# Kernel tuning notes

Measured on AMD Instinct MI355X. Metric: run time of the kernel, lower is better.

## Reference

```python
import jax, jax.numpy as jnp
import numpy as np

B, C, N = 2, 1024, 80
D = 3 * C + 2  # 3074 token dim
DFF = 2048     # torch TransformerEncoderLayer default dim_feedforward
HW = 224
REFINE = 3
EPS = 1e-5


def _layernorm(x, g, b):
    m = jnp.mean(x, axis=-1, keepdims=True)
    v = jnp.mean((x - m) ** 2, axis=-1, keepdims=True)
    return g * (x - m) / jnp.sqrt(v + EPS) + b


def _pos_encoding(seq_len, dim):
    pos = jnp.arange(seq_len, dtype=jnp.float32)[:, None]
    div = jnp.exp(jnp.arange(0, dim, 2, dtype=jnp.float32) * (-np.log(10000.0) / dim))
    pe = jnp.zeros((seq_len, dim), dtype=jnp.float32)
    pe = pe.at[:, 0::2].set(jnp.sin(pos * div)).at[:, 1::2].set(jnp.cos(pos * div))
    return pe


def _forward(pre_f, curr_f, first_f, ln_g, ln_b, ipw, ipb, opw, opb,
             n1g, n1b, l1w, l1b, l2w, l2b, n2g, n2b, ow, ob,
             prev_b, first_b):
    # --- vectorized find_best_shift: batched circular L1 correlation ---
    idx = (jnp.arange(N)[None, :] - jnp.arange(N)[:, None]) % N  # [shift, pos]
    rolled = first_b[:, idx]                                     # [B, N, N, 2]
    dist = jnp.abs(prev_b[:, None] - rolled).sum(axis=(-1, -2))  # [B, N]
    best = jnp.argmin(dist, axis=1)                              # first min, like torch loop
    roll_idx = (jnp.arange(N)[None, :] - best[:, None]) % N      # [B, N]
    first_b = jax.vmap(lambda fb, ri: fb[ri])(first_b, roll_idx)

    # --- bilinear upsample to 224x224 (F.interpolate, align_corners=False) ---
    up = lambda f: jax.image.resize(f, (f.shape[0], f.shape[1], HW, HW), method='bilinear')
    pre_up, curr_up, first_up = up(pre_f), up(curr_f), up(first_f)

    # --- vectorized get_bou_features: [B,N,C] gather ---
    gather = jax.vmap(lambda f, b: f[:, b[:, 0], b[:, 1]].T)
    pre_q = gather(pre_up, prev_b)      # [B, N, C]
    first_q = gather(first_up, first_b)  # [B, N, C]

    pe = _pos_encoding(N, D)
    curr = prev_b.astype(jnp.float32)
    scale = 1.0 / jnp.sqrt(jnp.float32(D))
    results = []
    for _ in range(REFINE):
        bf = gather(curr_up, curr.astype(jnp.int32))          # [B, N, C]
        tokens = jnp.concatenate([pre_q, bf, curr, first_q], axis=-1)  # [B, N, D]
        tokens = _layernorm(tokens, ln_g, ln_b)
        tokens = tokens + pe[None]
        # --- TransformerEncoderLayer (post-norm, nhead=1, relu, eval/no dropout) ---
        qkv = tokens @ ipw.T + ipb
        q, k, v = jnp.split(qkv, 3, axis=-1)
        attn = jax.nn.softmax(jnp.einsum('bqd,bkd->bqk', q, k) * scale, axis=-1)
        a = jnp.einsum('bqk,bkd->bqd', attn, v) @ opw.T + opb
        x = _layernorm(tokens + a, n1g, n1b)
        ff = jax.nn.relu(x @ l1w.T + l1b) @ l2w.T + l2b
        x = _layernorm(x + ff, n2g, n2b)
        out = x @ ow.T + ob                                   # [B, N, 1026]
        curr = jnp.clip(curr + out[..., C:], 0.0, 223.0)
        pre_q = pre_q + out[..., :C]
        results.append(curr)
    return jnp.stack(results)  # [REFINE, B, N, 2]


def setup_inputs() -> dict:
    key = jax.random.key(0)
    ks = jax.random.split(key, 12)
    f = lambda i, s: jax.random.normal(ks[i], s, dtype=jnp.float32)
    w = lambda i, s: 0.02 * jax.random.normal(ks[i], s, dtype=jnp.float32)
    return {
        'pre_img_features': f(0, (B, C, 14, 14)),
        'curr_img_features': f(1, (B, C, 14, 14)),
        'first_img_features': f(2, (B, C, 14, 14)),
        'previous_boundary': jax.random.randint(ks[3], (B, N, 2), 0, HW),
        'first_boundary': jax.random.randint(ks[4], (B, N, 2), 0, HW),
        'ln_g': jnp.ones((D,), jnp.float32), 'ln_b': jnp.zeros((D,), jnp.float32),
        'in_proj_w': w(5, (3 * D, D)), 'in_proj_b': jnp.zeros((3 * D,), jnp.float32),
        'out_proj_w': w(6, (D, D)), 'out_proj_b': jnp.zeros((D,), jnp.float32),
        'norm1_g': jnp.ones((D,), jnp.float32), 'norm1_b': jnp.zeros((D,), jnp.float32),
        'lin1_w': w(7, (DFF, D)), 'lin1_b': jnp.zeros((DFF,), jnp.float32),
        'lin2_w': w(8, (D, DFF)), 'lin2_b': jnp.zeros((D,), jnp.float32),
        'norm2_g': jnp.ones((D,), jnp.float32), 'norm2_b': jnp.zeros((D,), jnp.float32),
        'out_w': w(9, (C + 2, D)), 'out_b': jnp.zeros((C + 2,), jnp.float32),
    }


def reference(pre_img_features, curr_img_features, first_img_features,
              previous_boundary, first_boundary,
              ln_g, ln_b, in_proj_w, in_proj_b, out_proj_w, out_proj_b,
              norm1_g, norm1_b, lin1_w, lin1_b, lin2_w, lin2_b,
              norm2_g, norm2_b, out_w, out_b):
    return _forward(pre_img_features, curr_img_features, first_img_features,
                    ln_g, ln_b, in_proj_w, in_proj_b, out_proj_w, out_proj_b,
                    norm1_g, norm1_b, lin1_w, lin1_b, lin2_w, lin2_b,
                    norm2_g, norm2_b, out_w, out_b,
                    previous_boundary, first_boundary)
```

## Files before the change

### kernel.cpp

```cpp
#include <hip/hip_runtime.h>
#include <math.h>

#define B_    2
#define C_    1024
#define N_    80
#define D_    3074
#define DFF_  2048
#define OD_   1026
#define QKV_  9222
#define M_    160
#define EPS_  1e-5f
#define KPD_  3104

#define SQKV 4
#define PQKV 25
#define SOP  8
#define POP  13
#define SFF1 11
#define PFF1 9
#define SFF2 8
#define PFF2 8
#define SHD  11
#define PHD  9

typedef __attribute__((ext_vector_type(8))) short bf16x8;
typedef __attribute__((ext_vector_type(4))) float f32x4;

__device__ inline short f2bf(float f) {
    unsigned u = __float_as_uint(f);
    u += 0x7fffu + ((u >> 16) & 1u);
    return (short)(u >> 16);
}

__device__ inline int pack2bf(float lo, float hi) {
    return (int)(unsigned short)f2bf(lo) | ((int)(unsigned short)f2bf(hi) << 16);
}

__device__ inline float wave_sum(float v) {
#pragma unroll
    for (int off = 32; off > 0; off >>= 1) v += __shfl_down(v, off, 64);
    return v;
}

__device__ inline void block_reduce_2(float& s, float& s2, float* red) {
    int tid = threadIdx.x;
    int lane = tid & 63, wid = tid >> 6;
    s = wave_sum(s);
    s2 = wave_sum(s2);
    if (lane == 0) { red[wid] = s; red[4 + wid] = s2; }
    __syncthreads();
    if (tid == 0) {
        red[8] = red[0] + red[1] + red[2] + red[3];
        red[9] = red[4] + red[5] + red[6] + red[7];
    }
    __syncthreads();
    s = red[8]; s2 = red[9];
}

__device__ inline void bilin_setup(int p, int& i0, int& i1, float& t) {
    float s = (p + 0.5f) * 0.0625f - 0.5f;
    s = fminf(fmaxf(s, 0.0f), 13.0f);
    i0 = (int)s;
    t = s - (float)i0;
    i1 = min(i0 + 1, 13);
}

__device__ inline float bilin_tap(const float* f, int y0, int y1, float ty,
                                  int x0, int x1, float tx) {
    float a = f[y0 * 14 + x0], b = f[y0 * 14 + x1];
    float c = f[y1 * 14 + x0], d = f[y1 * 14 + x1];
    return (1.f - ty) * ((1.f - tx) * a + tx * b) + ty * ((1.f - tx) * c + tx * d);
}

__global__ __launch_bounds__(128) void align_kernel(const int* __restrict__ prev_b,
                                                    const int* __restrict__ first_b,
                                                    int* __restrict__ fb_al) {
    int b = blockIdx.x;
    int tid = threadIdx.x;
    __shared__ int dist[N_];
    __shared__ int bestIdx;
    if (tid < N_) {
        int s = 0;
        for (int j = 0; j < N_; ++j) {
            int src = (j - tid) % N_;
            if (src < 0) src += N_;
            int dy = prev_b[(b * N_ + j) * 2] - first_b[(b * N_ + src) * 2];
            int dx = prev_b[(b * N_ + j) * 2 + 1] - first_b[(b * N_ + src) * 2 + 1];
            s += abs(dy) + abs(dx);
        }
        dist[tid] = s;
    }
    __syncthreads();
    if (tid == 0) {
        int best = 0, bd = dist[0];
        for (int i = 1; i < N_; ++i)
            if (dist[i] < bd) { bd = dist[i]; best = i; }
        bestIdx = best;
    }
    __syncthreads();
    if (tid < N_) {
        int src = (tid - bestIdx) % N_;
        if (src < 0) src += N_;
        fb_al[(b * N_ + tid) * 2]     = first_b[(b * N_ + src) * 2];
        fb_al[(b * N_ + tid) * 2 + 1] = first_b[(b * N_ + src) * 2 + 1];
    }
}

__global__ __launch_bounds__(256) void gather_init_kernel(
        const float* __restrict__ pre_f, const float* __restrict__ first_f,
        const int* __restrict__ prev_b, const int* __restrict__ fb_al,
        float* __restrict__ pre_q, float* __restrict__ first_q,
        float* __restrict__ curr) {
    int m = blockIdx.x;
    int b = m / N_;
    int tid = threadIdx.x;
    int py = prev_b[m * 2], px = prev_b[m * 2 + 1];
    int fy = fb_al[m * 2], fx = fb_al[m * 2 + 1];
    int py0, py1, px0, px1, fy0, fy1, fx0, fx1;
    float pty, ptx, fty, ftx;
    bilin_setup(py, py0, py1, pty);
    bilin_setup(px, px0, px1, ptx);
    bilin_setup(fy, fy0, fy1, fty);
    bilin_setup(fx, fx0, fx1, ftx);
    for (int c = tid; c < C_; c += 256) {
        const float* fp = pre_f + (size_t)(b * C_ + c) * 196;
        const float* ff = first_f + (size_t)(b * C_ + c) * 196;
        pre_q[(size_t)m * C_ + c]   = bilin_tap(fp, py0, py1, pty, px0, px1, ptx);
        first_q[(size_t)m * C_ + c] = bilin_tap(ff, fy0, fy1, fty, fx0, fx1, ftx);
    }
    if (tid < 2) curr[m * 2 + tid] = (float)prev_b[m * 2 + tid];
}

__global__ __launch_bounds__(256) void pe_kernel(float* __restrict__ pe) {
    int n = blockIdx.x;
    const float negLogDivD = -logf(10000.0f) / (float)D_;
    for (int d = threadIdx.x; d < D_; d += 256) {
        int kk = d >> 1;
        float ang = (float)n * expf((float)(2 * kk) * negLogDivD);
        pe[(size_t)n * D_ + d] = (d & 1) ? cosf(ang) : sinf(ang);
    }
}

__global__ __launch_bounds__(256) void tokens_kernel(
        const float* __restrict__ curr_f, const float* __restrict__ pre_q,
        const float* __restrict__ first_q, const float* __restrict__ curr,
        const float* __restrict__ ln_g, const float* __restrict__ ln_b,
        const float* __restrict__ pe_tab,
        float* __restrict__ tokens, short* __restrict__ tokens_bf) {
    int m = blockIdx.x;
    int b = m / N_;
    int n = m % N_;
    int tid = threadIdx.x;
    __shared__ float bf[C_];
    __shared__ float red[10];

    float cy = curr[m * 2], cx = curr[m * 2 + 1];
    int iy = (int)cy, ix = (int)cx;
    int y0, y1, x0, x1;
    float ty, tx;
    bilin_setup(iy, y0, y1, ty);
    bilin_setup(ix, x0, x1, tx);
    for (int c = tid; c < C_; c += 256) {
        const float* f = curr_f + (size_t)(b * C_ + c) * 196;
        bf[c] = bilin_tap(f, y0, y1, ty, x0, x1, tx);
    }
    __syncthreads();

    float s = 0.f, s2 = 0.f;
    for (int d = tid; d < D_; d += 256) {
        float v;
        if (d < C_)            v = pre_q[(size_t)m * C_ + d];
        else if (d < 2 * C_)   v = bf[d - C_];
        else if (d == 2 * C_)  v = cy;
        else if (d == 2*C_+1)  v = cx;
        else                   v = first_q[(size_t)m * C_ + (d - 2 * C_ - 2)];
        s += v; s2 += v * v;
    }
    block_reduce_2(s, s2, red);
    float mean = s / (float)D_;
    float var = s2 / (float)D_ - mean * mean;
    float inv = rsqrtf(var + EPS_);

    for (int d = tid; d < KPD_; d += 256) {
        if (d < D_) {
            float v;
            if (d < C_)            v = pre_q[(size_t)m * C_ + d];
            else if (d < 2 * C_)   v = bf[d - C_];
            else if (d == 2 * C_)  v = cy;
            else if (d == 2*C_+1)  v = cx;
            else                   v = first_q[(size_t)m * C_ + (d - 2 * C_ - 2)];
            float ln = ln_g[d] * (v - mean) * inv + ln_b[d];
            float val = ln + pe_tab[(size_t)n * D_ + d];
            tokens[(size_t)m * D_ + d] = val;
            tokens_bf[(size_t)m * KPD_ + d] = f2bf(val);
        } else {
            tokens_bf[(size_t)m * KPD_ + d] = 0;
        }
    }
}

__global__ __launch_bounds__(256) void wpack2(const float* __restrict__ w,
                                              short* __restrict__ o,
                                              int K, int O, int nch, int ntiles) {
    int gw = (int)((blockIdx.x * 256 + threadIdx.x) >> 6);
    if (gw >= ntiles) return;
    int lane = threadIdx.x & 63;
    int strip = gw / nch, chunk = gw - strip * nch;
    int row = strip * 16 + (lane >> 2);
    int k0 = chunk * 32 + (lane & 3) * 8;
    float f[8];
    if (row < O && k0 + 8 <= K) {
        const float* src = w + (size_t)row * K + k0;
        float2 a = *(const float2*)(src);
        float2 b = *(const float2*)(src + 2);
        float2 c = *(const float2*)(src + 4);
        float2 d = *(const float2*)(src + 6);
        f[0]=a.x; f[1]=a.y; f[2]=b.x; f[3]=b.y;
        f[4]=c.x; f[5]=c.y; f[6]=d.x; f[7]=d.y;
    } else {
#pragma unroll
        for (int j = 0; j < 8; ++j) {
            int k = k0 + j;
            f[j] = (row < O && k < K) ? w[(size_t)row * K + k] : 0.f;
        }
    }
    int p0 = pack2bf(f[0], f[1]);
    int p1 = pack2bf(f[2], f[3]);
    int p2 = pack2bf(f[4], f[5]);
    int p3 = pack2bf(f[6], f[7]);
    int src = (lane & 15) * 4 + (lane >> 4);
    int4 out;
    out.x = __shfl(p0, src, 64);
    out.y = __shfl(p1, src, 64);
    out.z = __shfl(p2, src, 64);
    out.w = __shfl(p3, src, 64);
    *(int4*)(o + (size_t)gw * 512 + (size_t)lane * 8) = out;
}

template <int SW>
__global__ __launch_bounds__(512) void gemm_stage(
        const short* __restrict__ A, const short* __restrict__ Wp,
        const float* __restrict__ bias, float* __restrict__ part,
        int KpA, int nch, int O, int per) {
    int cs = blockIdx.y * per;
    int ce = min(nch, cs + per);
    if (cs >= ce) return;
    int tid = threadIdx.x;
    int lane = tid & 63, wave = tid >> 6;
    int col = lane & 15, quad = lane >> 4;
    int s0 = (blockIdx.x * 8 + wave) * SW;

    __shared__ short lbuf[2][160 * 32];

    int m0 = tid >> 2, p8 = (tid & 3) * 8;
    int m1 = (tid + 512) >> 2;
    const short* a0 = A + (size_t)m0 * KpA + p8;
    const short* a1 = A + (size_t)m1 * KpA + p8;
    bf16x8 sr0, sr1;

    f32x4 acc[SW][10];
#pragma unroll
    for (int j = 0; j < SW; ++j)
#pragma unroll
        for (int t = 0; t < 10; ++t)
#pragma unroll
            for (int r = 0; r < 4; ++r) acc[j][t][r] = 0.f;

    const short* wbase[SW];
#pragma unroll
    for (int j = 0; j < SW; ++j)
        wbase[j] = Wp + (size_t)(s0 + j) * nch * 512 + (size_t)lane * 8;
    bf16x8 wc[SW], wn[SW];

    sr0 = *(const bf16x8*)(a0 + (size_t)cs * 32);
    if (tid < 128) sr1 = *(const bf16x8*)(a1 + (size_t)cs * 32);
#pragma unroll
    for (int j = 0; j < SW; ++j)
        wc[j] = *(const bf16x8*)(wbase[j] + (size_t)cs * 512);
    *(bf16x8*)(&lbuf[0][m0 * 32 + p8]) = sr0;
    if (tid < 128) *(bf16x8*)(&lbuf[0][m1 * 32 + p8]) = sr1;
    __syncthreads();

    int cur = 0;
    for (int c = cs; c < ce; ++c) {
        bool more = (c + 1) < ce;
        if (more) {
            sr0 = *(const bf16x8*)(a0 + (size_t)(c + 1) * 32);
            if (tid < 128) sr1 = *(const bf16x8*)(a1 + (size_t)(c + 1) * 32);
#pragma unroll
            for (int j = 0; j < SW; ++j)
                wn[j] = *(const bf16x8*)(wbase[j] + (size_t)(c + 1) * 512);
        }
#pragma unroll
        for (int t = 0; t < 10; ++t) {
            bf16x8 af = *(const bf16x8*)(&lbuf[cur][t * 512 + col * 32 + quad * 8]);
#pragma unroll
            for (int j = 0; j < SW; ++j)
                acc[j][t] = __builtin_amdgcn_mfma_f32_16x16x32_bf16(af, wc[j], acc[j][t], 0, 0, 0);
        }
        if (more) {
            *(bf16x8*)(&lbuf[cur ^ 1][m0 * 32 + p8]) = sr0;
            if (tid < 128) *(bf16x8*)(&lbuf[cur ^ 1][m1 * 32 + p8]) = sr1;
        }
        __syncthreads();
#pragma unroll
        for (int j = 0; j < SW; ++j) wc[j] = wn[j];
        cur ^= 1;
    }

    float* pout = part + (size_t)blockIdx.y * M_ * O;
#pragma unroll
    for (int j = 0; j < SW; ++j) {
        int oc = (s0 + j) * 16 + col;
        if (oc < O) {
            float bv = (blockIdx.y == 0) ? bias[oc] : 0.f;
#pragma unroll
            for (int t = 0; t < 10; ++t)
#pragma unroll
                for (int r = 0; r < 4; ++r)
                    pout[(size_t)(t * 16 + quad * 4 + r) * O + oc] = acc[j][t][r] + bv;
        }
    }
}

__global__ __launch_bounds__(256) void gemm_mfma_sk(
        const short* __restrict__ A, const float* __restrict__ Wf,
        const float* __restrict__ bias, float* __restrict__ Cout,
        int K, int KpA, int O, int KC) {
    int kc0 = blockIdx.y * KC;
    if (kc0 >= K) return;
    int kend = min(K, kc0 + KC);

    int lane = threadIdx.x & 63;
    int wave = threadIdx.x >> 6;
    int col  = lane & 15;
    int quad = lane >> 4;
    int o0 = blockIdx.x * 128 + wave * 32 + col;
    int o1 = o0 + 16;
    int oc0 = min(o0, O - 1), oc1 = min(o1, O - 1);

    const float* wrow0 = Wf + (size_t)oc0 * K + quad * 8;
    const float* wrow1 = Wf + (size_t)oc1 * K + quad * 8;
    const short* abase = A + (size_t)col * KpA + quad * 8;

    f32x4 acc0[10], acc1[10];
#pragma unroll
    for (int t = 0; t < 10; ++t)
#pragma unroll
        for (int r = 0; r < 4; ++r) { acc0[t][r] = 0.f; acc1[t][r] = 0.f; }

    int nfull = (kend - kc0) >> 5;
    bf16x8 aCur[10];
    float2 wCur[8];
    if (nfull > 0) {
#pragma unroll
        for (int t = 0; t < 10; ++t)
            aCur[t] = *(const bf16x8*)(abase + (size_t)t * 16 * KpA + kc0);
#pragma unroll
        for (int j = 0; j < 4; ++j) {
            wCur[j]     = *(const float2*)(wrow0 + kc0 + 2 * j);
            wCur[4 + j] = *(const float2*)(wrow1 + kc0 + 2 * j);
        }
    }
    for (int i = 0; i < nfull; ++i) {
        bf16x8 aNxt[10];
        float2 wNxt[8];
        if (i + 1 < nfull) {
            int kn = kc0 + (i + 1) * 32;
#pragma unroll
            for (int t = 0; t < 10; ++t)
                aNxt[t] = *(const bf16x8*)(abase + (size_t)t * 16 * KpA + kn);
#pragma unroll
            for (int j = 0; j < 4; ++j) {
                wNxt[j]     = *(const float2*)(wrow0 + kn + 2 * j);
                wNxt[4 + j] = *(const float2*)(wrow1 + kn + 2 * j);
            }
        }
        bf16x8 b0, b1;
#pragma unroll
        for (int j = 0; j < 4; ++j) {
            b0[2*j] = f2bf(wCur[j].x);     b0[2*j+1] = f2bf(wCur[j].y);
            b1[2*j] = f2bf(wCur[4+j].x);   b1[2*j+1] = f2bf(wCur[4+j].y);
        }
#pragma unroll
        for (int t = 0; t < 10; ++t) {
            acc0[t] = __builtin_amdgcn_mfma_f32_16x16x32_bf16(aCur[t], b0, acc0[t], 0, 0, 0);
            acc1[t] = __builtin_amdgcn_mfma_f32_16x16x32_bf16(aCur[t], b1, acc1[t], 0, 0, 0);
        }
#pragma unroll
        for (int t = 0; t < 10; ++t) aCur[t] = aNxt[t];
#pragma unroll
        for (int j = 0; j < 8; ++j) wCur[j] = wNxt[j];
    }
    int kmain = kc0 + nfull * 32;
    if (kmain < kend) {
        bf16x8 b0, b1;
#pragma unroll
        for (int j = 0; j < 8; ++j) {
            int k = kmain + quad * 8 + j;
            b0[j] = (k < kend) ? f2bf(Wf[(size_t)oc0 * K + k]) : (short)0;
            b1[j] = (k < kend) ? f2bf(Wf[(size_t)oc1 * K + k]) : (short)0;
        }
#pragma unroll
        for (int t = 0; t < 10; ++t) {
            bf16x8 af = *(const bf16x8*)(abase + (size_t)t * 16 * KpA + kmain);
            acc0[t] = __builtin_amdgcn_mfma_f32_16x16x32_bf16(af, b0, acc0[t], 0, 0, 0);
            acc1[t] = __builtin_amdgcn_mfma_f32_16x16x32_bf16(af, b1, acc1[t], 0, 0, 0);
        }
    }
    if (o0 < O) {
        float bv = (blockIdx.y == 0) ? bias[o0] : 0.f;
#pragma unroll
        for (int t = 0; t < 10; ++t)
#pragma unroll
            for (int r = 0; r < 4; ++r)
                atomicAdd(&Cout[(size_t)(t * 16 + quad * 4 + r) * O + o0], acc0[t][r] + bv);
    }
    if (o1 < O) {
        float bv = (blockIdx.y == 0) ? bias[o1] : 0.f;
#pragma unroll
        for (int t = 0; t < 10; ++t)
#pragma unroll
            for (int r = 0; r < 4; ++r)
                atomicAdd(&Cout[(size_t)(t * 16 + quad * 4 + r) * O + o1], acc1[t][r] + bv);
    }
}

__global__ __launch_bounds__(256) void relu_cvt_kernel(const float* __restrict__ in,
                                                       int S, size_t sstr,
                                                       short* __restrict__ out,
                                                       int n) {
    int i = blockIdx.x * 256 + threadIdx.x;
    if (i < n) {
        float v = 0.f;
        for (int s = 0; s < S; ++s) v += in[(size_t)s * sstr + i];
        out[i] = f2bf(fmaxf(v, 0.f));
    }
}

__global__ __launch_bounds__(256) void qkv_cvt_kernel(const float* __restrict__ part,
                                                      int S,
                                                      short* __restrict__ q_bf,
                                                      short* __restrict__ k_bf,
                                                      short* __restrict__ v_bf) {
    int mb = blockIdx.x;
    int b = mb / 96, q = mb % 96;
    if (q >= N_) {
        for (int d = threadIdx.x; d < KPD_; d += 256)
            v_bf[((size_t)b * 96 + q) * KPD_ + d] = 0;
        return;
    }
    int m = b * N_ + q;
    for (int d = threadIdx.x; d < KPD_; d += 256) {
        short qv = 0, kv = 0, vv = 0;
        if (d < D_) {
            float qf = 0.f, kf = 0.f, vf = 0.f;
            for (int s = 0; s < S; ++s) {
                const float* p = part + (size_t)s * M_ * QKV_ + (size_t)m * QKV_;
                qf += p[d]; kf += p[D_ + d]; vf += p[2 * D_ + d];
            }
            qv = f2bf(qf); kv = f2bf(kf); vv = f2bf(vf);
        }
        q_bf[(size_t)m * KPD_ + d] = qv;
        k_bf[(size_t)m * KPD_ + d] = kv;
        v_bf[((size_t)b * 96 + q) * KPD_ + d] = vv;
    }
}

__global__ __launch_bounds__(256) void attn_sc(const short* __restrict__ q_bf,
                                               const short* __restrict__ k_bf,
                                               short* __restrict__ p_bf) {
    int bi = blockIdx.x;
    int b = bi / 5, qt = bi % 5;
    int lane = threadIdx.x & 63, wave = threadIdx.x >> 6;
    int col = lane & 15, quad = lane >> 4;
    const short* qbase = q_bf + (size_t)(b * N_ + qt * 16 + col) * KPD_ + quad * 8;
    const short* kb = k_bf + (size_t)(b * N_ + col) * KPD_ + quad * 8;

    f32x4 acc[5];
#pragma unroll
    for (int kt = 0; kt < 5; ++kt)
#pragma unroll
        for (int r = 0; r < 4; ++r) acc[kt][r] = 0.f;

    int c0 = wave * 25, c1 = min(97, c0 + 25);
    for (int c = c0; c < c1; ++c) {
        bf16x8 af = *(const bf16x8*)(qbase + (size_t)c * 32);
#pragma unroll
        for (int kt = 0; kt < 5; ++kt) {
            bf16x8 kf = *(const bf16x8*)(kb + (size_t)(kt * 16) * KPD_ + (size_t)c * 32);
            acc[kt] = __builtin_amdgcn_mfma_f32_16x16x32_bf16(af, kf, acc[kt], 0, 0, 0);
        }
    }

    __shared__ f32x4 red[4][5][64];
    __shared__ float sl[16][80];
#pragma unroll
    for (int kt = 0; kt < 5; ++kt) red[wave][kt][lane] = acc[kt];
    __syncthreads();
    float scale = rsqrtf((float)D_);
    for (int item = threadIdx.x; item < 320; item += 256) {
        int kt = item >> 6, l2 = item & 63;
        int c2 = l2 & 15, q2 = l2 >> 4;
        f32x4 v = red[0][kt][l2];
#pragma unroll
        for (int w = 1; w < 4; ++w)
#pragma unroll
            for (int r = 0; r < 4; ++r) v[r] += red[w][kt][l2][r];
#pragma unroll
        for (int r = 0; r < 4; ++r)
            sl[q2 * 4 + r][kt * 16 + c2] = v[r] * scale;
    }
    __syncthreads();

    int r = wave * 4 + (lane >> 4);
    int cb = lane & 15;
    float v[5];
    float mx = -1e30f;
#pragma unroll
    for (int i = 0; i < 5; ++i) { v[i] = sl[r][cb + 16 * i]; mx = fmaxf(mx, v[i]); }
#pragma unroll
    for (int off = 1; off < 16; off <<= 1) mx = fmaxf(mx, __shfl_xor(mx, off, 64));
    float e[5];
    float sum = 0.f;
#pragma unroll
    for (int i = 0; i < 5; ++i) { e[i] = expf(v[i] - mx); sum += e[i]; }
#pragma unroll
    for (int off = 1; off < 16; off <<= 1) sum += __shfl_xor(sum, off, 64);
    float rs = 1.0f / sum;
    size_t m96 = (size_t)(b * N_ + qt * 16 + r) * 96;
#pragma unroll
    for (int i = 0; i < 5; ++i) p_bf[m96 + cb + 16 * i] = f2bf(e[i] * rs);
    p_bf[m96 + 80 + cb] = 0;
}

__global__ __launch_bounds__(256) void av_mfma(const short* __restrict__ p_bf,
                                               const short* __restrict__ v_bf,
                                               short* __restrict__ av_bf) {
    int bi = blockIdx.x;
    int b = bi / 49, g = bi % 49;
    int lane = threadIdx.x & 63, wave = threadIdx.x >> 6;
    int dtile = g * 4 + wave;
    if (dtile >= 194) return;
    int d0 = dtile * 16;
    int col = lane & 15, quad = lane >> 4;
    const short* pbase = p_bf + (size_t)b * N_ * 96 + quad * 8;
    const short* vb = v_bf + (size_t)b * 96 * KPD_ + d0 + col;
    f32x4 acc[5];
#pragma unroll
    for (int t = 0; t < 5; ++t)
#pragma unroll
        for (int r = 0; r < 4; ++r) acc[t][r] = 0.f;
#pragma unroll
    for (int c = 0; c < 3; ++c) {
        bf16x8 bf8;
#pragma unroll
        for (int j = 0; j < 8; ++j)
            bf8[j] = vb[(size_t)(c * 32 + quad * 8 + j) * KPD_];
#pragma unroll
        for (int t = 0; t < 5; ++t) {
            bf16x8 af = *(const bf16x8*)(pbase + (size_t)(t * 16 + col) * 96 + c * 32);
            acc[t] = __builtin_amdgcn_mfma_f32_16x16x32_bf16(af, bf8, acc[t], 0, 0, 0);
        }
    }
#pragma unroll
    for (int t = 0; t < 5; ++t)
#pragma unroll
        for (int r = 0; r < 4; ++r)
            av_bf[(size_t)(b * N_ + t * 16 + quad * 4 + r) * KPD_ + d0 + col] = f2bf(acc[t][r]);
}

template <bool WF32>
__global__ __launch_bounds__(256) void ln_kernel(const float* __restrict__ xin,
                                                 int S, size_t sstr,
                                                 const float* __restrict__ res,
                                                 const float* __restrict__ g,
                                                 const float* __restrict__ bta,
                                                 float* __restrict__ outf,
                                                 short* __restrict__ outb) {
    int m = blockIdx.x;
    int tid = threadIdx.x;
    __shared__ float red[10];
    const float* xr = xin + (size_t)m * D_;
    const float* rr = res + (size_t)m * D_;
    float vv[13];
    float s = 0.f, s2 = 0.f;
#pragma unroll
    for (int i = 0; i < 13; ++i) {
        int d = tid + i * 256;
        float v = 0.f;
        if (d < D_) {
            v = rr[d];
            for (int sp = 0; sp < S; ++sp) v += xr[(size_t)sp * sstr + d];
            s += v; s2 += v * v;
        }
        vv[i] = v;
    }
    block_reduce_2(s, s2, red);
    float mean = s / (float)D_;
    float var = s2 / (float)D_ - mean * mean;
    float inv = rsqrtf(var + EPS_);
#pragma unroll
    for (int i = 0; i < 13; ++i) {
        int d = tid + i * 256;
        if (d < D_) {
            float y = g[d] * (vv[i] - mean) * inv + bta[d];
            if (WF32) outf[(size_t)m * D_ + d] = y;
            outb[(size_t)m * KPD_ + d] = f2bf(y);
        } else if (d < KPD_) {
            outb[(size_t)m * KPD_ + d] = 0;
        }
    }
}

__global__ __launch_bounds__(256) void update_kernel(const float* __restrict__ part,
                                                     int S, size_t sstr,
                                                     float* __restrict__ curr,
                                                     float* __restrict__ pre_q,
                                                     float* __restrict__ results) {
    int m = blockIdx.x;
    int tid = threadIdx.x;
    const float* pr = part + (size_t)m * OD_;
    for (int c = tid; c < C_; c += 256) {
        float v = 0.f;
        for (int s = 0; s < S; ++s) v += pr[(size_t)s * sstr + c];
        pre_q[(size_t)m * C_ + c] += v;
    }
    if (tid < 2) {
        float v = 0.f;
        for (int s = 0; s < S; ++s) v += pr[(size_t)s * sstr + C_ + tid];
        float nc = curr[m * 2 + tid] + v;
        nc = fminf(fmaxf(nc, 0.f), 223.f);
        curr[m * 2 + tid] = nc;
        results[m * 2 + tid] = nc;
    }
}

extern "C" void kernel_launch(void* const* d_in, const int* in_sizes, int n_in,
                              void* d_out, int out_size, void* d_ws, size_t ws_size,
                              hipStream_t stream) {
    const float* pre_f   = (const float*)d_in[0];
    const float* curr_f  = (const float*)d_in[1];
    const float* first_f = (const float*)d_in[2];
    const int*   prev_b  = (const int*)d_in[3];
    const int*   first_b = (const int*)d_in[4];
    const float* ln_g    = (const float*)d_in[5];
    const float* ln_b    = (const float*)d_in[6];
    const float* ipw     = (const float*)d_in[7];
    const float* ipb     = (const float*)d_in[8];
    const float* opw     = (const float*)d_in[9];
    const float* opb     = (const float*)d_in[10];
    const float* n1g     = (const float*)d_in[11];
    const float* n1b     = (const float*)d_in[12];
    const float* l1w     = (const float*)d_in[13];
    const float* l1b     = (const float*)d_in[14];
    const float* l2w     = (const float*)d_in[15];
    const float* l2b     = (const float*)d_in[16];
    const float* n2g     = (const float*)d_in[17];
    const float* n2b     = (const float*)d_in[18];
    const float* ow      = (const float*)d_in[19];
    const float* ob      = (const float*)d_in[20];
    float* outp = (float*)d_out;

    float* wf = (float*)d_ws;
    size_t off = 0;
    int*   fb_al   = (int*)(wf + off); off += 320;
    float* curr    = wf + off;         off += 320;
    float* pre_q   = wf + off;         off += (size_t)M_ * C_;
    float* first_q = wf + off;         off += (size_t)M_ * C_;
    float* tokens  = wf + off;         off += (size_t)M_ * D_;
    float* xbuf    = wf + off;         off += (size_t)M_ * D_;
    float* pe_tab  = wf + off;         off += (size_t)N_ * D_;
    short* tokens_bf = (short*)(wf + off); off += (size_t)M_ * KPD_ / 2;
    short* x_bf      = (short*)(wf + off); off += (size_t)M_ * KPD_ / 2;
    short* x2_bf     = (short*)(wf + off); off += (size_t)M_ * KPD_ / 2;
    short* av_bf     = (short*)(wf + off); off += (size_t)M_ * KPD_ / 2;
    short* ff1_bf    = (short*)(wf + off); off += (size_t)M_ * DFF_ / 2;
    short* q_bf      = (short*)(wf + off); off += (size_t)M_ * KPD_ / 2;
    short* k_bf      = (short*)(wf + off); off += (size_t)M_ * KPD_ / 2;
    short* v_bf      = (short*)(wf + off); off += (size_t)B_ * 96 * KPD_ / 2;
    short* p_bf      = (short*)(wf + off); off += (size_t)M_ * 96 / 2;
    size_t commonF = off;

    size_t o2 = commonF;
    short* ipw_p2 = (short*)(wf + o2); o2 += (size_t)592 * 97 * 256;
    short* opw_p2 = (short*)(wf + o2); o2 += (size_t)208 * 97 * 256;
    short* l1w_p2 = (short*)(wf + o2); o2 += (size_t)128 * 97 * 256;
    short* l2w_p2 = (short*)(wf + o2); o2 += (size_t)208 * 64 * 256;
    short* ow_p2  = (short*)(wf + o2); o2 += (size_t)80  * 97 * 256;
    float* gpart  = wf + o2;           o2 += (size_t)SQKV * M_ * QKV_;

    size_t o0 = commonF;
    float* qkv   = wf + o0; o0 += (size_t)M_ * QKV_;
    float* aout  = wf + o0; o0 += (size_t)M_ * D_;
    float* ff1f  = wf + o0; o0 += (size_t)M_ * DFF_;
    float* ffout = wf + o0; o0 += (size_t)M_ * D_;
    float* outb  = wf + o0; o0 += (size_t)M_ * OD_;

    int tier = (ws_size >= o2 * sizeof(float)) ? 2 : 0;
    (void)in_sizes; (void)n_in; (void)out_size;

    hipLaunchKernelGGL(align_kernel, dim3(B_), dim3(128), 0, stream,
                       prev_b, first_b, fb_al);
    hipLaunchKernelGGL(gather_init_kernel, dim3(M_), dim3(256), 0, stream,
                       pre_f, first_f, prev_b, fb_al, pre_q, first_q, curr);
    hipLaunchKernelGGL(pe_kernel, dim3(N_), dim3(256), 0, stream, pe_tab);

    if (tier == 2) {
        hipLaunchKernelGGL(wpack2, dim3(592 * 97 / 4), dim3(256), 0, stream,
                           ipw, ipw_p2, D_, QKV_, 97, 592 * 97);
        hipLaunchKernelGGL(wpack2, dim3(208 * 97 / 4), dim3(256), 0, stream,
                           opw, opw_p2, D_, D_, 97, 208 * 97);
        hipLaunchKernelGGL(wpack2, dim3(128 * 97 / 4), dim3(256), 0, stream,
                           l1w, l1w_p2, D_, DFF_, 97, 128 * 97);
        hipLaunchKernelGGL(wpack2, dim3(208 * 64 / 4), dim3(256), 0, stream,
                           l2w, l2w_p2, DFF_, D_, 64, 208 * 64);
        hipLaunchKernelGGL(wpack2, dim3(80 * 97 / 4), dim3(256), 0, stream,
                           ow, ow_p2, D_, OD_, 97, 80 * 97);
    }

    for (int it = 0; it < 3; ++it) {
        if (tier == 0) {
            hipMemsetAsync(qkv,   0, (size_t)M_ * QKV_ * 4, stream);
            hipMemsetAsync(aout,  0, (size_t)M_ * D_   * 4, stream);
            hipMemsetAsync(ff1f,  0, (size_t)M_ * DFF_ * 4, stream);
            hipMemsetAsync(ffout, 0, (size_t)M_ * D_   * 4, stream);
            hipMemsetAsync(outb,  0, (size_t)M_ * OD_  * 4, stream);
        }

        hipLaunchKernelGGL(tokens_kernel, dim3(M_), dim3(256), 0, stream,
                           curr_f, pre_q, first_q, curr, ln_g, ln_b, pe_tab,
                           tokens, tokens_bf);
        if (tier == 2)
            hipLaunchKernelGGL((gemm_stage<2>), dim3(37, SQKV), dim3(512), 0, stream,
                               tokens_bf, ipw_p2, ipb, gpart, KPD_, 97, QKV_, PQKV);
        else
            hipLaunchKernelGGL(gemm_mfma_sk, dim3(73, 6), dim3(256), 0, stream,
                               tokens_bf, ipw, ipb, qkv, D_, KPD_, QKV_, 544);
        hipLaunchKernelGGL(qkv_cvt_kernel, dim3(B_ * 96), dim3(256), 0, stream,
                           (tier == 2) ? gpart : qkv, (tier == 2) ? SQKV : 1,
                           q_bf, k_bf, v_bf);
        hipLaunchKernelGGL(attn_sc, dim3(B_ * 5), dim3(256), 0, stream,
                           q_bf, k_bf, p_bf);
        hipLaunchKernelGGL(av_mfma, dim3(98), dim3(256), 0, stream,
                           p_bf, v_bf, av_bf);
        if (tier == 2)
            hipLaunchKernelGGL((gemm_stage<2>), dim3(13, SOP), dim3(512), 0, stream,
                               av_bf, opw_p2, opb, gpart, KPD_, 97, D_, POP);
        else
            hipLaunchKernelGGL(gemm_mfma_sk, dim3(25, 10), dim3(256), 0, stream,
                               av_bf, opw, opb, aout, D_, KPD_, D_, 320);
        hipLaunchKernelGGL((ln_kernel<true>), dim3(M_), dim3(256), 0, stream,
                           (tier == 2) ? gpart : aout, (tier == 2) ? SOP : 1, (size_t)M_ * D_,
                           tokens, n1g, n1b, xbuf, x_bf);
        if (tier == 2)
            hipLaunchKernelGGL((gemm_stage<2>), dim3(8, SFF1), dim3(512), 0, stream,
                               x_bf, l1w_p2, l1b, gpart, KPD_, 97, DFF_, PFF1);
        else
            hipLaunchKernelGGL(gemm_mfma_sk, dim3(16, 17), dim3(256), 0, stream,
                               x_bf, l1w, l1b, ff1f, D_, KPD_, DFF_, 192);
        hipLaunchKernelGGL(relu_cvt_kernel, dim3((M_ * DFF_ + 255) / 256), dim3(256), 0, stream,
                           (tier == 2) ? gpart : ff1f, (tier == 2) ? SFF1 : 1, (size_t)M_ * DFF_,
                           ff1_bf, M_ * DFF_);
        if (tier == 2)
            hipLaunchKernelGGL((gemm_stage<2>), dim3(13, SFF2), dim3(512), 0, stream,
                               ff1_bf, l2w_p2, l2b, gpart, DFF_, 64, D_, PFF2);
        else
            hipLaunchKernelGGL(gemm_mfma_sk, dim3(25, 11), dim3(256), 0, stream,
                               ff1_bf, l2w, l2b, ffout, DFF_, DFF_, D_, 192);
        hipLaunchKernelGGL((ln_kernel<false>), dim3(M_), dim3(256), 0, stream,
                           (tier == 2) ? gpart : ffout, (tier == 2) ? SFF2 : 1, (size_t)M_ * D_,
                           xbuf, n2g, n2b, (float*)nullptr, x2_bf);
        if (tier == 2)
            hipLaunchKernelGGL((gemm_stage<2>), dim3(5, SHD), dim3(512), 0, stream,
                               x2_bf, ow_p2, ob, gpart, KPD_, 97, OD_, PHD);
        else
            hipLaunchKernelGGL(gemm_mfma_sk, dim3(9, 13), dim3(256), 0, stream,
                               x2_bf, ow, ob, outb, D_, KPD_, OD_, 256);
        hipLaunchKernelGGL(update_kernel, dim3(M_), dim3(256), 0, stream,
                           (tier == 2) ? gpart : outb, (tier == 2) ? SHD : 1, (size_t)M_ * OD_,
                           curr, pre_q, outp + (size_t)it * M_ * 2);
    }
}
```

Baseline: 1.022 ms.

## Fuse QKV GEMM with bf16 conversion, merge softmax and AV, retune split-K

Replaces the split-K QKV GEMM and its separate reduce/convert kernel with one non-split kernel that writes bf16 Q/K/V directly with bias. Merges the softmax-score kernel and the AV multiply into one kernel that keeps probabilities in shared memory. Retunes the split-K factors of the other GEMMs, caches token values in registers inside the layernorm kernel, and zeroes the padding once up front. The QKV GEMM now runs on only 74 blocks with full K per block, which trades split-K parallelism for fewer launches and less partial-sum traffic. The fused attention runs on only 10 blocks.

Measured after the change: 1.171 ms. +14.6%, slower.

```diff
diff --git a/kernel.cpp b/kernel.cpp
--- a/kernel.cpp
+++ b/kernel.cpp
@@ -12,16 +12,14 @@
 #define EPS_  1e-5f
 #define KPD_  3104
 
-#define SQKV 4
-#define PQKV 25
-#define SOP  8
-#define POP  13
-#define SFF1 11
-#define PFF1 9
-#define SFF2 8
-#define PFF2 8
-#define SHD  11
-#define PHD  9
+#define SOP  6
+#define POP  17
+#define SFF1 6
+#define PFF1 17
+#define SFF2 6
+#define PFF2 11
+#define SHD  6
+#define PHD  17
 
 typedef __attribute__((ext_vector_type(8))) short bf16x8;
 typedef __attribute__((ext_vector_type(4))) float f32x4;
@@ -141,6 +139,27 @@
     }
 }
 
+__global__ __launch_bounds__(64) void zero_pads(short* __restrict__ q_bf,
+                                                short* __restrict__ k_bf,
+                                                short* __restrict__ v_bf) {
+    int bi = blockIdx.x;
+    int tid = threadIdx.x;
+    if (bi < M_) {
+        int b = bi / N_, q = bi % N_;
+        int d = D_ + tid;
+        if (d < KPD_) {
+            q_bf[(size_t)bi * KPD_ + d] = 0;
+            k_bf[(size_t)bi * KPD_ + d] = 0;
+            v_bf[((size_t)b * 96 + q) * KPD_ + d] = 0;
+        }
+    } else {
+        int r = bi - M_;
+        int b = r / 16, q = 80 + (r % 16);
+        for (int d = tid; d < KPD_; d += 64)
+            v_bf[((size_t)b * 96 + q) * KPD_ + d] = 0;
+    }
+}
+
 __global__ __launch_bounds__(256) void tokens_kernel(
         const float* __restrict__ curr_f, const float* __restrict__ pre_q,
         const float* __restrict__ first_q, const float* __restrict__ curr,
@@ -166,34 +185,36 @@
     }
     __syncthreads();
 
+    float vv[13];
     float s = 0.f, s2 = 0.f;
-    for (int d = tid; d < D_; d += 256) {
-        float v;
-        if (d < C_)            v = pre_q[(size_t)m * C_ + d];
-        else if (d < 2 * C_)   v = bf[d - C_];
-        else if (d == 2 * C_)  v = cy;
-        else if (d == 2*C_+1)  v = cx;
-        else                   v = first_q[(size_t)m * C_ + (d - 2 * C_ - 2)];
-        s += v; s2 += v * v;
-    }
-    block_reduce_2(s, s2, red);
-    float mean = s / (float)D_;
-    float var = s2 / (float)D_ - mean * mean;
-    float inv = rsqrtf(var + EPS_);
-
-    for (int d = tid; d < KPD_; d += 256) {
+#pragma unroll
+    for (int i = 0; i < 13; ++i) {
+        int d = tid + i * 256;
+        float v = 0.f;
         if (d < D_) {
-            float v;
             if (d < C_)            v = pre_q[(size_t)m * C_ + d];
             else if (d < 2 * C_)   v = bf[d - C_];
             else if (d == 2 * C_)  v = cy;
             else if (d == 2*C_+1)  v = cx;
             else                   v = first_q[(size_t)m * C_ + (d - 2 * C_ - 2)];
-            float ln = ln_g[d] * (v - mean) * inv + ln_b[d];
+            s += v; s2 += v * v;
+        }
+        vv[i] = v;
+    }
+    block_reduce_2(s, s2, red);
+    float mean = s / (float)D_;
+    float var = s2 / (float)D_ - mean * mean;
+    float inv = rsqrtf(var + EPS_);
+
+#pragma unroll
+    for (int i = 0; i < 13; ++i) {
+        int d = tid + i * 256;
+        if (d < D_) {
+            float ln = ln_g[d] * (vv[i] - mean) * inv + ln_b[d];
             float val = ln + pe_tab[(size_t)n * D_ + d];
             tokens[(size_t)m * D_ + d] = val;
             tokens_bf[(size_t)m * KPD_ + d] = f2bf(val);
-        } else {
+        } else if (d < KPD_) {
             tokens_bf[(size_t)m * KPD_ + d] = 0;
         }
     }
@@ -237,6 +258,103 @@
     *(int4*)(o + (size_t)gw * 512 + (size_t)lane * 8) = out;
 }
 
+__global__ __launch_bounds__(256) void gemm_qkv_fused(
+        const short* __restrict__ A, const short* __restrict__ Wp,
+        const float* __restrict__ bias,
+        short* __restrict__ q_bf, short* __restrict__ k_bf,
+        short* __restrict__ v_bf) {
+    const int nch = 97;
+    int tid = threadIdx.x;
+    int lane = tid & 63, wave = tid >> 6;
+    int col = lane & 15, quad = lane >> 4;
+    int s0 = (blockIdx.x * 4 + wave) * 2;
+
+    __shared__ short lbuf[2][160 * 32];
+
+    int m0 = tid >> 2, p8 = (tid & 3) * 8;
+    int m1 = (tid + 256) >> 2;
+    int m2 = (tid + 512) >> 2;
+    const short* a0 = A + (size_t)m0 * KPD_ + p8;
+    const short* a1 = A + (size_t)m1 * KPD_ + p8;
+    const short* a2 = A + (size_t)m2 * KPD_ + p8;
+    bf16x8 sr0, sr1, sr2;
+
+    f32x4 acc[2][10];
+#pragma unroll
+    for (int j = 0; j < 2; ++j)
+#pragma unroll
+        for (int t = 0; t < 10; ++t)
+#pragma unroll
+            for (int r = 0; r < 4; ++r) acc[j][t][r] = 0.f;
+
+    const short* wbase[2];
+#pragma unroll
+    for (int j = 0; j < 2; ++j)
+        wbase[j] = Wp + (size_t)(s0 + j) * nch * 512 + (size_t)lane * 8;
+    bf16x8 wc[2], wn[2];
+
+    sr0 = *(const bf16x8*)(a0);
+    sr1 = *(const bf16x8*)(a1);
+    if (tid < 128) sr2 = *(const bf16x8*)(a2);
+#pragma unroll
+    for (int j = 0; j < 2; ++j) wc[j] = *(const bf16x8*)(wbase[j]);
+    *(bf16x8*)(&lbuf[0][m0 * 32 + p8]) = sr0;
+    *(bf16x8*)(&lbuf[0][m1 * 32 + p8]) = sr1;
+    if (tid < 128) *(bf16x8*)(&lbuf[0][m2 * 32 + p8]) = sr2;
+    __syncthreads();
+
+    int cur = 0;
+    for (int c = 0; c < nch; ++c) {
+        bool more = (c + 1) < nch;
+        if (more) {
+            sr0 = *(const bf16x8*)(a0 + (size_t)(c + 1) * 32);
+            sr1 = *(const bf16x8*)(a1 + (size_t)(c + 1) * 32);
+            if (tid < 128) sr2 = *(const bf16x8*)(a2 + (size_t)(c + 1) * 32);
+#pragma unroll
+            for (int j = 0; j < 2; ++j)
+                wn[j] = *(const bf16x8*)(wbase[j] + (size_t)(c + 1) * 512);
+        }
+#pragma unroll
+        for (int t = 0; t < 10; ++t) {
+            bf16x8 af = *(const bf16x8*)(&lbuf[cur][t * 512 + col * 32 + quad * 8]);
+#pragma unroll
+            for (int j = 0; j < 2; ++j)
+                acc[j][t] = __builtin_amdgcn_mfma_f32_16x16x32_bf16(af, wc[j], acc[j][t], 0, 0, 0);
+        }
+        if (more) {
+            *(bf16x8*)(&lbuf[cur ^ 1][m0 * 32 + p8]) = sr0;
+            *(bf16x8*)(&lbuf[cur ^ 1][m1 * 32 + p8]) = sr1;
+            if (tid < 128) *(bf16x8*)(&lbuf[cur ^ 1][m2 * 32 + p8]) = sr2;
+        }
+        __syncthreads();
+#pragma unroll
+        for (int j = 0; j < 2; ++j) wc[j] = wn[j];
+        cur ^= 1;
+    }
+
+#pragma unroll
+    for (int j = 0; j < 2; ++j) {
+        int oc = (s0 + j) * 16 + col;
+        if (oc < QKV_) {
+            float bv = bias[oc];
+            short* dp;
+            int dcol;
+            bool isv = false;
+            if (oc < D_)            { dp = q_bf; dcol = oc; }
+            else if (oc < 2 * D_)   { dp = k_bf; dcol = oc - D_; }
+            else                    { dp = v_bf; dcol = oc - 2 * D_; isv = true; }
+#pragma unroll
+            for (int t = 0; t < 10; ++t)
+#pragma unroll
+                for (int r = 0; r < 4; ++r) {
+                    int m = t * 16 + quad * 4 + r;
+                    int rr = isv ? (m + ((m >= N_) ? 16 : 0)) : m;
+                    dp[(size_t)rr * KPD_ + dcol] = f2bf(acc[j][t][r] + bv);
+                }
+        }
+    }
+}
+
 template <int SW>
 __global__ __launch_bounds__(512) void gemm_stage(
         const short* __restrict__ A, const short* __restrict__ Wp,
@@ -438,38 +556,27 @@
     }
 }
 
-__global__ __launch_bounds__(256) void qkv_cvt_kernel(const float* __restrict__ part,
-                                                      int S,
+__global__ __launch_bounds__(256) void qkv_cvt_kernel(const float* __restrict__ qkv,
                                                       short* __restrict__ q_bf,
                                                       short* __restrict__ k_bf,
                                                       short* __restrict__ v_bf) {
-    int mb = blockIdx.x;
-    int b = mb / 96, q = mb % 96;
-    if (q >= N_) {
-        for (int d = threadIdx.x; d < KPD_; d += 256)
-            v_bf[((size_t)b * 96 + q) * KPD_ + d] = 0;
-        return;
-    }
-    int m = b * N_ + q;
+    int m = blockIdx.x;
+    int b = m / N_, q = m % N_;
+    const float* src = qkv + (size_t)m * QKV_;
     for (int d = threadIdx.x; d < KPD_; d += 256) {
-        short qv = 0, kv = 0, vv = 0;
-        if (d < D_) {
-            float qf = 0.f, kf = 0.f, vf = 0.f;
-            for (int s = 0; s < S; ++s) {
-                const float* p = part + (size_t)s * M_ * QKV_ + (size_t)m * QKV_;
-                qf += p[d]; kf += p[D_ + d]; vf += p[2 * D_ + d];
-            }
-            qv = f2bf(qf); kv = f2bf(kf); vv = f2bf(vf);
-        }
+        short qv = (d < D_) ? f2bf(src[d])          : (short)0;
+        short kv = (d < D_) ? f2bf(src[D_ + d])     : (short)0;
+        short vv = (d < D_) ? f2bf(src[2 * D_ + d]) : (short)0;
         q_bf[(size_t)m * KPD_ + d] = qv;
         k_bf[(size_t)m * KPD_ + d] = kv;
         v_bf[((size_t)b * 96 + q) * KPD_ + d] = vv;
     }
 }
 
-__global__ __launch_bounds__(256) void attn_sc(const short* __restrict__ q_bf,
+__global__ __launch_bounds__(256) void attn_av(const short* __restrict__ q_bf,
                                                const short* __restrict__ k_bf,
-                                               short* __restrict__ p_bf) {
+                                               const short* __restrict__ v_bf,
+                                               short* __restrict__ av_bf) {
     int bi = blockIdx.x;
     int b = bi / 5, qt = bi % 5;
     int lane = threadIdx.x & 63, wave = threadIdx.x >> 6;
@@ -495,6 +602,7 @@
 
     __shared__ f32x4 red[4][5][64];
     __shared__ float sl[16][80];
+    __shared__ short p_s[16][104];
 #pragma unroll
     for (int kt = 0; kt < 5; ++kt) red[wave][kt][lane] = acc[kt];
     __syncthreads();
@@ -513,61 +621,49 @@
     }
     __syncthreads();
 
-    int r = wave * 4 + (lane >> 4);
-    int cb = lane & 15;
-    float v[5];
-    float mx = -1e30f;
-#pragma unroll
-    for (int i = 0; i < 5; ++i) { v[i] = sl[r][cb + 16 * i]; mx = fmaxf(mx, v[i]); }
-#pragma unroll
-    for (int off = 1; off < 16; off <<= 1) mx = fmaxf(mx, __shfl_xor(mx, off, 64));
-    float e[5];
-    float sum = 0.f;
-#pragma unroll
-    for (int i = 0; i < 5; ++i) { e[i] = expf(v[i] - mx); sum += e[i]; }
-#pragma unroll
-    for (int off = 1; off < 16; off <<= 1) sum += __shfl_xor(sum, off, 64);
-    float rs = 1.0f / sum;
-    size_t m96 = (size_t)(b * N_ + qt * 16 + r) * 96;
-#pragma unroll
-    for (int i = 0; i < 5; ++i) p_bf[m96 + cb + 16 * i] = f2bf(e[i] * rs);
-    p_bf[m96 + 80 + cb] = 0;
-}
-
-__global__ __launch_bounds__(256) void av_mfma(const short* __restrict__ p_bf,
-                                               const short* __restrict__ v_bf,
-                                               short* __restrict__ av_bf) {
-    int bi = blockIdx.x;
-    int b = bi / 49, g = bi % 49;
-    int lane = threadIdx.x & 63, wave = threadIdx.x >> 6;
-    int dtile = g * 4 + wave;
-    if (dtile >= 194) return;
-    int d0 = dtile * 16;
-    int col = lane & 15, quad = lane >> 4;
-    const short* pbase = p_bf + (size_t)b * N_ * 96 + quad * 8;
-    const short* vb = v_bf + (size_t)b * 96 * KPD_ + d0 + col;
-    f32x4 acc[5];
-#pragma unroll
-    for (int t = 0; t < 5; ++t)
-#pragma unroll
-        for (int r = 0; r < 4; ++r) acc[t][r] = 0.f;
-#pragma unroll
-    for (int c = 0; c < 3; ++c) {
-        bf16x8 bf8;
-#pragma unroll
-        for (int j = 0; j < 8; ++j)
-            bf8[j] = vb[(size_t)(c * 32 + quad * 8 + j) * KPD_];
-#pragma unroll
-        for (int t = 0; t < 5; ++t) {
-            bf16x8 af = *(const bf16x8*)(pbase + (size_t)(t * 16 + col) * 96 + c * 32);
-            acc[t] = __builtin_amdgcn_mfma_f32_16x16x32_bf16(af, bf8, acc[t], 0, 0, 0);
-        }
-    }
-#pragma unroll
-    for (int t = 0; t < 5; ++t)
+    {
+        int r = wave * 4 + (lane >> 4);
+        int cb = lane & 15;
+        float v[5];
+        float mx = -1e30f;
+#pragma unroll
+        for (int i = 0; i < 5; ++i) { v[i] = sl[r][cb + 16 * i]; mx = fmaxf(mx, v[i]); }
+#pragma unroll
+        for (int off = 1; off < 16; off <<= 1) mx = fmaxf(mx, __shfl_xor(mx, off, 64));
+        float e[5];
+        float sum = 0.f;
+#pragma unroll
+        for (int i = 0; i < 5; ++i) { e[i] = expf(v[i] - mx); sum += e[i]; }
+#pragma unroll
+        for (int off = 1; off < 16; off <<= 1) sum += __shfl_xor(sum, off, 64);
+        float rs = 1.0f / sum;
+#pragma unroll
+        for (int i = 0; i < 5; ++i) p_s[r][cb + 16 * i] = f2bf(e[i] * rs);
+        p_s[r][80 + cb] = 0;
+        if (cb < 8) p_s[r][96 + cb] = 0;
+    }
+    __syncthreads();
+
+    const short* vb0 = v_bf + (size_t)b * 96 * KPD_ + col;
+    for (int dt = wave; dt < 194; dt += 4) {
+        int d0 = dt * 16;
+        const short* vb = vb0 + d0;
+        f32x4 a2;
+#pragma unroll
+        for (int r = 0; r < 4; ++r) a2[r] = 0.f;
+#pragma unroll
+        for (int c = 0; c < 3; ++c) {
+            bf16x8 vf;
+#pragma unroll
+            for (int j = 0; j < 8; ++j)
+                vf[j] = vb[(size_t)(c * 32 + quad * 8 + j) * KPD_];
+            bf16x8 pf = *(const bf16x8*)(&p_s[col][c * 32 + quad * 8]);
+            a2 = __builtin_amdgcn_mfma_f32_16x16x32_bf16(pf, vf, a2, 0, 0, 0);
+        }
 #pragma unroll
         for (int r = 0; r < 4; ++r)
-            av_bf[(size_t)(b * N_ + t * 16 + quad * 4 + r) * KPD_ + d0 + col] = f2bf(acc[t][r]);
+            av_bf[(size_t)(b * N_ + qt * 16 + quad * 4 + r) * KPD_ + d0 + col] = f2bf(a2[r]);
+    }
 }
 
 template <bool WF32>
@@ -679,7 +775,6 @@
     short* q_bf      = (short*)(wf + off); off += (size_t)M_ * KPD_ / 2;
     short* k_bf      = (short*)(wf + off); off += (size_t)M_ * KPD_ / 2;
     short* v_bf      = (short*)(wf + off); off += (size_t)B_ * 96 * KPD_ / 2;
-    short* p_bf      = (short*)(wf + off); off += (size_t)M_ * 96 / 2;
     size_t commonF = off;
 
     size_t o2 = commonF;
@@ -688,7 +783,7 @@
     short* l1w_p2 = (short*)(wf + o2); o2 += (size_t)128 * 97 * 256;
     short* l2w_p2 = (short*)(wf + o2); o2 += (size_t)208 * 64 * 256;
     short* ow_p2  = (short*)(wf + o2); o2 += (size_t)80  * 97 * 256;
-    float* gpart  = wf + o2;           o2 += (size_t)SQKV * M_ * QKV_;
+    float* gpart  = wf + o2;           o2 += (size_t)6 * M_ * D_;
 
     size_t o0 = commonF;
     float* qkv   = wf + o0; o0 += (size_t)M_ * QKV_;
@@ -705,6 +800,8 @@
     hipLaunchKernelGGL(gather_init_kernel, dim3(M_), dim3(256), 0, stream,
                        pre_f, first_f, prev_b, fb_al, pre_q, first_q, curr);
     hipLaunchKernelGGL(pe_kernel, dim3(N_), dim3(256), 0, stream, pe_tab);
+    hipLaunchKernelGGL(zero_pads, dim3(M_ + 32), dim3(64), 0, stream,
+                       q_bf, k_bf, v_bf);
 
     if (tier == 2) {
         hipLaunchKernelGGL(wpack2, dim3(592 * 97 / 4), dim3(256), 0, stream,
@@ -731,19 +828,17 @@
         hipLaunchKernelGGL(tokens_kernel, dim3(M_), dim3(256), 0, stream,
                            curr_f, pre_q, first_q, curr, ln_g, ln_b, pe_tab,
                            tokens, tokens_bf);
-        if (tier == 2)
-            hipLaunchKernelGGL((gemm_stage<2>), dim3(37, SQKV), dim3(512), 0, stream,
-                               tokens_bf, ipw_p2, ipb, gpart, KPD_, 97, QKV_, PQKV);
-        else
+        if (tier == 2) {
+            hipLaunchKernelGGL(gemm_qkv_fused, dim3(74), dim3(256), 0, stream,
+                               tokens_bf, ipw_p2, ipb, q_bf, k_bf, v_bf);
+        } else {
             hipLaunchKernelGGL(gemm_mfma_sk, dim3(73, 6), dim3(256), 0, stream,
                                tokens_bf, ipw, ipb, qkv, D_, KPD_, QKV_, 544);
-        hipLaunchKernelGGL(qkv_cvt_kernel, dim3(B_ * 96), dim3(256), 0, stream,
-                           (tier == 2) ? gpart : qkv, (tier == 2) ? SQKV : 1,
-                           q_bf, k_bf, v_bf);
-        hipLaunchKernelGGL(attn_sc, dim3(B_ * 5), dim3(256), 0, stream,
-                           q_bf, k_bf, p_bf);
-        hipLaunchKernelGGL(av_mfma, dim3(98), dim3(256), 0, stream,
-                           p_bf, v_bf, av_bf);
+            hipLaunchKernelGGL(qkv_cvt_kernel, dim3(M_), dim3(256), 0, stream,
+                               qkv, q_bf, k_bf, v_bf);
+        }
+        hipLaunchKernelGGL(attn_av, dim3(B_ * 5), dim3(256), 0, stream,
+                           q_bf, k_bf, v_bf, av_bf);
         if (tier == 2)
             hipLaunchKernelGGL((gemm_stage<2>), dim3(13, SOP), dim3(512), 0, stream,
                                av_bf, opw_p2, opb, gpart, KPD_, 97, D_, POP);
```
